# Performance work log

Measured on AMD Instinct MI355X. Metric: run time of the kernel, lower is better.

## Reference

```python
import jax, jax.numpy as jnp
import numpy as np

N, B, D_IN, D_OUT, E = 1024, 128, 64, 64, 16


def setup_inputs() -> dict:
    key = jax.random.key(0)
    k1, k2, k3, k4 = jax.random.split(key, 4)
    x = jax.random.normal(k1, (B, N, D_IN), dtype=jnp.float32)
    node_embeddings = jax.random.normal(k2, (N, E), dtype=jnp.float32)
    weights_pool = jax.random.normal(k3, (E, D_IN, D_OUT), dtype=jnp.float32)
    bias_pool = jax.random.normal(k4, (E, D_OUT), dtype=jnp.float32)
    return {"x": x, "node_embeddings": node_embeddings,
            "weights_pool": weights_pool, "bias_pool": bias_pool}


def reference(x, node_embeddings, weights_pool, bias_pool):
    # Adaptive adjacency: softmax over rows of relu(E E^T), shape [N, N]
    scores = jax.nn.relu(node_embeddings @ node_embeddings.T)
    supports = jax.nn.softmax(scores, axis=1)
    # Per-node weights [N, D_IN, D_OUT] and bias [N, D_OUT]
    weights = jnp.einsum('nd,dio->nio', node_embeddings, weights_pool)
    bias = node_embeddings @ bias_pool  # [N, D_OUT]
    # Graph aggregation: [B, N, D_IN]
    x_g = jnp.einsum('nm,bmc->bnc', supports, x)
    # Per-node linear transform + bias: [B, N, D_OUT]
    x_gconv = jnp.einsum('bni,nio->bno', x_g, weights) + bias
    return x_gconv
```

## Files before the change

kernel.cpp:

```cpp
#include <hip/hip_runtime.h>

#define N_NODES 1024
#define BATCH   128
#define E_DIM   16


typedef __attribute__((ext_vector_type(8))) short bf16x8;
typedef __attribute__((ext_vector_type(4))) float f32x4;
typedef __attribute__((ext_vector_type(16))) float f32x16;

__device__ __forceinline__ unsigned short f2bf(float f) {
    union { float f; unsigned int u; } v; v.f = f;
    unsigned int u = v.u;
    u += 0x7FFFu + ((u >> 16) & 1u);
    return (unsigned short)(u >> 16);
}

__device__ __forceinline__ void gload_lds16(const void* g, void* l) {
    __builtin_amdgcn_global_load_lds(
        (const __attribute__((address_space(1))) unsigned int*)g,
        (__attribute__((address_space(3))) unsigned int*)l, 16, 0, 0);
}

__global__ __launch_bounds__(256) void k_prep(const float* __restrict__ x,
                                              const float* __restrict__ emb,
                                              const float* __restrict__ wpool,
                                              const float* __restrict__ bpool,
                                              unsigned short* __restrict__ xbt,
                                              unsigned short* __restrict__ sup,
                                              unsigned short* __restrict__ Wt,
                                              float* __restrict__ bias) {
    __shared__ __align__(16) char smem[49408];
    const int bid = blockIdx.x;
    const int t = threadIdx.x;

    if (bid < 2048) {
        unsigned short* xt = (unsigned short*)smem;
        const int b  = bid >> 4;
        const int kt64 = bid & 15;
        const int m0 = kt64 * 64;
        const int c  = t & 63, mr = t >> 6;
        const float* src = x + ((long)b * N_NODES + m0 + mr) * 64 + c;
#pragma unroll
        for (int i = 0; i < 16; ++i)
            xt[c * 72 + mr + i * 4] = f2bf(src[(long)i * 4 * 64]);
        __syncthreads();
        const int cc = t >> 2, mb = (t & 3) * 16;
        const int p  = b >> 1, jr = (b & 1) * 64 + cc;
        unsigned short* dst = xbt + (long)p * 131072 + (long)kt64 * 8192 + jr * 8;
        *(bf16x8*)(dst + ((t & 3) * 2 + 0) * 1024) = *(const bf16x8*)(&xt[cc * 72 + mb]);
        *(bf16x8*)(dst + ((t & 3) * 2 + 1) * 1024) = *(const bf16x8*)(&xt[cc * 72 + mb + 8]);
    } else if (bid < 2304) {
        float (*en)[E_DIM] = (float(*)[E_DIM])smem;
        float* wl = (float*)(smem + 256);
        unsigned short* st = (unsigned short*)(smem + 256 + 16384);
        const int n0 = (bid - 2048) * 4;
        if (t < 64) en[t >> 4][t & 15] = emb[(n0 + (t >> 4)) * E_DIM + (t & 15)];
        __syncthreads();
        for (int c = 0; c < 16; ++c) {
#pragma unroll
            for (int e = 0; e < E_DIM; ++e) wl[e * 256 + t] = wpool[e * 4096 + c * 256 + t];
            __syncthreads();
            const int d2 = (c >> 1) * 512 + (t & 63) * 8 + (c & 1) * 4 + (t >> 6);
#pragma unroll
            for (int nn = 0; nn < 4; ++nn) {
                float s = 0.f;
#pragma unroll
                for (int e = 0; e < E_DIM; ++e) s = fmaf(en[nn][e], wl[e * 256 + t], s);
                st[nn * 4096 + d2] = f2bf(s);
            }
            __syncthreads();
        }
        {
            const int nn = t >> 6, o = t & 63;
            float s = 0.f;
#pragma unroll
            for (int e = 0; e < E_DIM; ++e) s = fmaf(en[nn][e], bpool[e * 64 + o], s);
            bias[(n0 + nn) * 64 + o] = s;
        }
#pragma unroll
        for (int r = 0; r < 8; ++r) {
            const int q = r * 256 + t;
            *(bf16x8*)(Wt + (long)n0 * 4096 + q * 8) = *(const bf16x8*)&st[q * 8];
        }
    } else {
        float* en  = (float*)smem;
        float* red = (float*)(smem + 64);
        const int n = bid - 2304;
        if (t < E_DIM) en[t] = emb[n * E_DIM + t];
        __syncthreads();
        float sc[4];
        float mx = -1e30f;
#pragma unroll
        for (int r = 0; r < 4; ++r) {
            const float* em = &emb[(r * 256 + t) * E_DIM];
            float s = 0.f;
#pragma unroll
            for (int e = 0; e < E_DIM; ++e) s = fmaf(en[e], em[e], s);
            s = fmaxf(s, 0.f);
            sc[r] = s;
            mx = fmaxf(mx, s);
        }
#pragma unroll
        for (int o = 32; o > 0; o >>= 1) mx = fmaxf(mx, __shfl_xor(mx, o));
        if ((t & 63) == 0) red[t >> 6] = mx;
        __syncthreads();
        mx = fmaxf(fmaxf(red[0], red[1]), fmaxf(red[2], red[3]));
        float sum = 0.f;
#pragma unroll
        for (int r = 0; r < 4; ++r) { sc[r] = __expf(sc[r] - mx); sum += sc[r]; }
#pragma unroll
        for (int o = 32; o > 0; o >>= 1) sum += __shfl_xor(sum, o);
        __syncthreads();
        if ((t & 63) == 0) red[t >> 6] = sum;
        __syncthreads();
        sum = red[0] + red[1] + red[2] + red[3];
        const float inv = 1.f / sum;
#pragma unroll
        for (int r = 0; r < 4; ++r) {
            const int m = r * 256 + t;
            const int off = (n >> 7) * 131072 + (m >> 6) * 8192 + ((m >> 3) & 7) * 1024
                          + (n & 127) * 8 + (m & 7);
            sup[off] = f2bf(sc[r] * inv);
        }
    }
}

__global__ __launch_bounds__(256, 2) void k_agg(const unsigned short* __restrict__ S,
                                                const unsigned short* __restrict__ Bt,
                                                unsigned short* __restrict__ xg) {
    __shared__ __align__(16) char lds[65536];
    const int t = threadIdx.x;
    const int lane = t & 63, wid = t >> 6;

    const int hw   = blockIdx.x + 8 * blockIdx.y;
    const int work = (hw & 7) * 64 + (hw >> 3);
    const int n0 = (work & 7) * 128, j0 = (work >> 3) * 128;
    const int wr = wid >> 1, wc = wid & 1;

    f32x16 acc[2][2];
#pragma unroll
    for (int m = 0; m < 2; ++m)
#pragma unroll
        for (int n = 0; n < 2; ++n)
#pragma unroll
            for (int r = 0; r < 16; ++r) acc[m][n][r] = 0.f;

    const unsigned short* pA = S  + (n0 >> 7) * 131072 + lane * 8;
    const unsigned short* pB = Bt + (j0 >> 7) * 131072 + lane * 8;
    const unsigned short* sp[4];
    int doff[4];
#pragma unroll
    for (int i = 0; i < 4; ++i) {
        const int c = wid * 4 + i;
        if (c < 8) { sp[i] = pA + c * 512;       doff[i] = c * 1024; }
        else       { sp[i] = pB + (c - 8) * 512; doff[i] = 8192 + (c - 8) * 1024; }
    }
#define STAGE(kt) do {                                                   \
        char* buf_ = lds + ((kt) & 3) * 16384;                           \
        const int ko_ = (kt) * 4096;                                     \
        gload_lds16(sp[0] + ko_, buf_ + doff[0]);                        \
        gload_lds16(sp[1] + ko_, buf_ + doff[1]);                        \
        gload_lds16(sp[2] + ko_, buf_ + doff[2]);                        \
        gload_lds16(sp[3] + ko_, buf_ + doff[3]);                        \
    } while (0)

    int aoff[2], boff[2];
#pragma unroll
    for (int m = 0; m < 2; ++m)
        aoff[m] = (lane >> 5) * 2048 + (wr * 64 + m * 32 + (lane & 31)) * 16;
#pragma unroll
    for (int n = 0; n < 2; ++n)
        boff[n] = 8192 + (lane >> 5) * 2048 + (wc * 64 + n * 32 + (lane & 31)) * 16;

    STAGE(0); STAGE(1);
    for (int kt = 0; kt < 32; ++kt) {
        if (kt < 31) asm volatile("s_waitcnt vmcnt(4)" ::: "memory");
        else         asm volatile("s_waitcnt vmcnt(0)" ::: "memory");
        __builtin_amdgcn_s_barrier();
        asm volatile("" ::: "memory");
        __builtin_amdgcn_sched_barrier(0);
        if (kt + 2 < 32) STAGE(kt + 2);
        const char* cur = lds + (kt & 3) * 16384;
        __builtin_amdgcn_s_setprio(1);
#pragma unroll
        for (int s = 0; s < 2; ++s) {
            bf16x8 a[2], b[2];
#pragma unroll
            for (int m = 0; m < 2; ++m) a[m] = *(const bf16x8*)(cur + s * 4096 + aoff[m]);
#pragma unroll
            for (int n = 0; n < 2; ++n) b[n] = *(const bf16x8*)(cur + s * 4096 + boff[n]);
#pragma unroll
            for (int m = 0; m < 2; ++m)
#pragma unroll
                for (int n = 0; n < 2; ++n)
                    acc[m][n] = __builtin_amdgcn_mfma_f32_32x32x16_bf16(a[m], b[n], acc[m][n], 0, 0, 0);
        }
        __builtin_amdgcn_s_setprio(0);
        asm volatile("" ::: "memory");
        __builtin_amdgcn_sched_barrier(0);
    }
#undef STAGE
    __syncthreads();

    char* lb = lds;
#pragma unroll
    for (int m = 0; m < 2; ++m) {
#pragma unroll
        for (int n = 0; n < 2; ++n) {
            const int col  = wc * 64 + n * 32 + (lane & 31);
            const int rowb = wr * 64 + m * 32 + 4 * (lane >> 5);
#pragma unroll
            for (int r = 0; r < 16; ++r) {
                const int row = rowb + (r & 3) + 8 * (r >> 2);
                *(unsigned short*)(lb + row * 256 + ((col * 2) ^ ((row & 7) << 4))) =
                    f2bf(acc[m][n][r]);
            }
        }
    }
    __syncthreads();
#pragma unroll
    for (int i = 0; i < 8; ++i) {
        const int idx = i * 256 + t;
        const int row = idx >> 4, cc = idx & 15;
        bf16x8 v = *(const bf16x8*)(lb + row * 256 + ((cc * 16) ^ ((row & 7) << 4)));
        const long dst = (long)(n0 + row) * 8192 + (cc & 7) * 1024
                       + ((j0 >> 6) + (cc >> 3)) * 8;
        *(bf16x8*)(xg + dst) = v;
    }
}

__global__ __launch_bounds__(256) void k_out(const unsigned short* __restrict__ xg,
                                             const unsigned short* __restrict__ Wt,
                                             const float* __restrict__ bias,
                                             float* __restrict__ out) {
    __shared__ __align__(16) char lds[49152];
    const int t = threadIdx.x, lane = t & 63, wid = t >> 6;
    const int nb = blockIdx.x * 2;
#pragma unroll
    for (int i = 0; i < 12; ++i) {
        const int c = wid * 12 + i;
        if (c < 32) {
            const int nn = c >> 4, k = c & 15;
            gload_lds16(xg + (long)(nb + nn) * 8192 + k * 512 + lane * 8,
                        lds + nn * 16384 + k * 1024);
        } else {
            const int cc = c - 32, nn = cc >> 3, k = cc & 7;
            gload_lds16(Wt + (long)(nb + nn) * 4096 + k * 512 + lane * 8,
                        lds + 32768 + nn * 8192 + k * 1024);
        }
    }
    __syncthreads();

    const int node = nb + (wid >> 1);
    const int bh   = wid & 1;
    const char* xl = lds + (wid >> 1) * 16384;
    const char* wlp = lds + 32768 + (wid >> 1) * 8192;

    f32x4 acc[4][4];
#pragma unroll
    for (int m = 0; m < 4; ++m)
#pragma unroll
        for (int n = 0; n < 4; ++n) acc[m][n] = f32x4{0.f, 0.f, 0.f, 0.f};

#pragma unroll
    for (int s = 0; s < 2; ++s) {
        const int kb = s * 4 + (lane >> 4);
        bf16x8 a[4], b[4];
#pragma unroll
        for (int m = 0; m < 4; ++m)
            a[m] = *(const bf16x8*)(xl + kb * 2048 + (bh * 64 + m * 16 + (lane & 15)) * 16);
#pragma unroll
        for (int n = 0; n < 4; ++n)
            b[n] = *(const bf16x8*)(wlp + kb * 1024 + (n * 16 + (lane & 15)) * 16);
#pragma unroll
        for (int m = 0; m < 4; ++m)
#pragma unroll
            for (int n = 0; n < 4; ++n)
                acc[m][n] = __builtin_amdgcn_mfma_f32_16x16x32_bf16(a[m], b[n], acc[m][n], 0, 0, 0);
    }

#pragma unroll
    for (int n = 0; n < 4; ++n) {
        const int o = n * 16 + (lane & 15);
        const float bv = bias[node * 64 + o];
#pragma unroll
        for (int m = 0; m < 4; ++m) {
            const int b0 = bh * 64 + m * 16 + (lane >> 4) * 4;
#pragma unroll
            for (int r = 0; r < 4; ++r)
                out[(long)(b0 + r) * 65536 + node * 64 + o] = acc[m][n][r] + bv;
        }
    }
}

extern "C" void kernel_launch(void* const* d_in, const int* in_sizes, int n_in,
                              void* d_out, int out_size, void* d_ws, size_t ws_size,
                              hipStream_t stream) {
    const float* x     = (const float*)d_in[0];
    const float* emb   = (const float*)d_in[1];
    const float* wpool = (const float*)d_in[2];
    const float* bpool = (const float*)d_in[3];
    float* out = (float*)d_out;

    char* ws = (char*)d_ws;
    unsigned short* sup  = (unsigned short*)(ws);
    unsigned short* xbt  = (unsigned short*)(ws + (2u  << 20));
    unsigned short* Wt   = (unsigned short*)(ws + (18u << 20));
    float*          bias = (float*)         (ws + (26u << 20));
    unsigned short* xg   = (unsigned short*)(ws + (27u << 20));
    (void)in_sizes; (void)n_in; (void)out_size; (void)ws_size;

    k_prep<<<dim3(3328), dim3(256), 0, stream>>>(x, emb, wpool, bpool,
                                                 xbt, sup, Wt, bias);
    k_agg<<<dim3(8, 64), dim3(256), 0, stream>>>(sup, xbt, xg);
    k_out<<<dim3(512), dim3(256), 0, stream>>>(xg, Wt, bias, out);
}
```

Before: 68.49 us.

## Transpose x directly from registers in prep and swizzle xg intermediate layout

The x-transpose part of the prep kernel no longer stages through LDS and a barrier; each thread gathers eight strided fp32 values, packs them into a bf16x8 vector and writes it straight to the blocked layout. The graph-aggregation epilogue now writes xg batch-major with an XOR swizzle on the k-block, so its global stores become more contiguous per node row. The output kernel's A-fragment LDS reads are changed to match that swizzle, which avoids bank conflicts. The cost is strided, less coalesced global reads of x in prep.

```diff
diff --git a/kernel.cpp b/kernel.cpp
--- a/kernel.cpp
+++ b/kernel.cpp
@@ -35,21 +35,19 @@
     const int t = threadIdx.x;
 
     if (bid < 2048) {
-        unsigned short* xt = (unsigned short*)smem;
-        const int b  = bid >> 4;
-        const int kt64 = bid & 15;
-        const int m0 = kt64 * 64;
-        const int c  = t & 63, mr = t >> 6;
-        const float* src = x + ((long)b * N_NODES + m0 + mr) * 64 + c;
-#pragma unroll
-        for (int i = 0; i < 16; ++i)
-            xt[c * 72 + mr + i * 4] = f2bf(src[(long)i * 4 * 64]);
-        __syncthreads();
-        const int cc = t >> 2, mb = (t & 3) * 16;
-        const int p  = b >> 1, jr = (b & 1) * 64 + cc;
-        unsigned short* dst = xbt + (long)p * 131072 + (long)kt64 * 8192 + jr * 8;
-        *(bf16x8*)(dst + ((t & 3) * 2 + 0) * 1024) = *(const bf16x8*)(&xt[cc * 72 + mb]);
-        *(bf16x8*)(dst + ((t & 3) * 2 + 1) * 1024) = *(const bf16x8*)(&xt[cc * 72 + mb + 8]);
+        const int b = bid >> 4, kt64 = bid & 15;
+        unsigned short* dstp = xbt + (long)(b >> 1) * 131072 + kt64 * 8192
+                             + (b & 1) * 512;
+#pragma unroll
+        for (int h = 0; h < 2; ++h) {
+            const int g = h * 256 + t;
+            const int kblk = g >> 6, c = g & 63;
+            const float* s = x + ((long)b * 1024 + kt64 * 64 + kblk * 8) * 64 + c;
+            bf16x8 r;
+#pragma unroll
+            for (int e = 0; e < 8; ++e) r[e] = (short)f2bf(s[e * 64]);
+            *(bf16x8*)(dstp + kblk * 1024 + c * 8) = r;
+        }
     } else if (bid < 2304) {
         float (*en)[E_DIM] = (float(*)[E_DIM])smem;
         float* wl = (float*)(smem + 256);
@@ -219,13 +217,14 @@
         }
     }
     __syncthreads();
+    const int b0 = j0 >> 6;
 #pragma unroll
     for (int i = 0; i < 8; ++i) {
         const int idx = i * 256 + t;
         const int row = idx >> 4, cc = idx & 15;
         bf16x8 v = *(const bf16x8*)(lb + row * 256 + ((cc * 16) ^ ((row & 7) << 4)));
-        const long dst = (long)(n0 + row) * 8192 + (cc & 7) * 1024
-                       + ((j0 >> 6) + (cc >> 3)) * 8;
+        const int b = b0 + (cc >> 3);
+        const long dst = (long)(n0 + row) * 8192 + b * 64 + ((cc & 7) ^ (b & 7)) * 8;
         *(bf16x8*)(xg + dst) = v;
     }
 }
@@ -268,8 +267,10 @@
         const int kb = s * 4 + (lane >> 4);
         bf16x8 a[4], b[4];
 #pragma unroll
-        for (int m = 0; m < 4; ++m)
-            a[m] = *(const bf16x8*)(xl + kb * 2048 + (bh * 64 + m * 16 + (lane & 15)) * 16);
+        for (int m = 0; m < 4; ++m) {
+            const int brow = bh * 64 + m * 16 + (lane & 15);
+            a[m] = *(const bf16x8*)(xl + brow * 128 + ((kb ^ (lane & 7)) << 4));
+        }
 #pragma unroll
         for (int n = 0; n < 4; ++n)
             b[n] = *(const bf16x8*)(wlp + kb * 1024 + (n * 16 + (lane & 15)) * 16);
```

Result: no change. 67.88 us (-0.9%).
